# Performance work log

Hardware: AMD Instinct MI355X
Metric: run time of the kernel (lower is better)

## Reference

```python
import jax, jax.numpy as jnp
import numpy as np

B, S, D = 2, 2048, 1024
N_EXP, TOP_K = 8, 2
CAP_FACTOR = 1.25

def setup_inputs() -> dict:
    key = jax.random.key(0)
    k1, k2 = jax.random.split(key)
    x = jax.random.normal(k1, (B, S, D), dtype=jnp.float32)
    W_gate = jax.random.normal(k2, (N_EXP, D), dtype=jnp.float32) * (1.0 / np.sqrt(D))
    return {"x": x, "W_gate": W_gate}

def reference(x, W_gate):
    Bq, Sq, d = x.shape
    N = Bq * Sq                      # num_tokens
    n_exp = W_gate.shape[0]
    top_k = TOP_K
    cap = int(N * top_k * CAP_FACTOR / n_exp)  # exp_capacity (static)

    x_flat = x.reshape(N, d)
    logits = x_flat @ W_gate.T                      # [N, n_exp]
    top_vals, top_idx = jax.lax.top_k(logits, top_k)  # [N, k]
    gates = jax.nn.softmax(top_vals, axis=-1)       # [N, k]

    # Serial token-major, k-minor assignment order == flatten row-major.
    e_flat = top_idx.reshape(-1)                    # [N*k]
    oh = jax.nn.one_hot(e_flat, n_exp, dtype=jnp.int32)
    # position within expert = # earlier slots routed to same expert
    pos = (jnp.cumsum(oh, axis=0) - oh)[jnp.arange(N * top_k), e_flat]
    pos_safe = jnp.where(pos < cap, pos, cap)       # cap -> out-of-bounds -> dropped

    tok = jnp.arange(N * top_k) // top_k            # owning token per slot
    g_flat = gates.reshape(-1)

    exp_mask = jnp.zeros((N, n_exp, cap), jnp.float32)
    exp_mask = exp_mask.at[tok, e_flat, pos_safe].set(g_flat, mode='drop')

    exp_batches = jnp.zeros((n_exp, cap, d), jnp.float32)
    exp_batches = exp_batches.at[e_flat, pos_safe].set(x_flat[tok], mode='drop')

    return gates, exp_mask, exp_batches
```

## Files before the change

kernel.cpp:

```cpp
#include <hip/hip_runtime.h>
#include <math.h>

#define NTOK   4096
#define DIM    1024
#define NEXP   8
#define CAP    1280

#define OUT_MASK_OFF   ((size_t)NTOK*2)
#define OUT_BATCH_OFF  (OUT_MASK_OFF + (size_t)NTOK*NEXP*CAP)

typedef float f4 __attribute__((ext_vector_type(4)));

__global__ __launch_bounds__(256) void gate_kernel(
    const float* __restrict__ x, const float* __restrict__ Wg,
    float* __restrict__ gates_out,
    int* __restrict__ e0a, int* __restrict__ e1a,
    float* __restrict__ g0a, float* __restrict__ g1a)
{
    const int wave = threadIdx.x >> 6;
    const int lane = threadIdx.x & 63;
    const int t    = blockIdx.x * 4 + wave;

    const f4* xr = (const f4*)(x + (size_t)t * DIM);
    f4 xv[4];
#pragma unroll
    for (int p = 0; p < 4; ++p) xv[p] = xr[p * 64 + lane];

    float acc[NEXP];
#pragma unroll
    for (int e = 0; e < NEXP; ++e) {
        const f4* wr = (const f4*)(Wg + (size_t)e * DIM);
        float a = 0.f;
#pragma unroll
        for (int p = 0; p < 4; ++p) {
            const f4 w = wr[p * 64 + lane];
            a += xv[p].x * w.x + xv[p].y * w.y + xv[p].z * w.z + xv[p].w * w.w;
        }
        acc[e] = a;
    }

#pragma unroll
    for (int off = 32; off >= 1; off >>= 1) {
#pragma unroll
        for (int e = 0; e < NEXP; ++e)
            acc[e] += __shfl_xor(acc[e], off);
    }

    if (lane == 0) {
        float best = -INFINITY, second = -INFINITY;
        int b0 = 0, b1 = 0;
#pragma unroll
        for (int e = 0; e < NEXP; ++e) {
            const float v = acc[e];
            if (v > best)        { second = best; b1 = b0; best = v; b0 = e; }
            else if (v > second) { second = v; b1 = e; }
        }
        const float e1v = __expf(second - best);
        const float inv = 1.0f / (1.0f + e1v);
        const float g0 = inv, g1 = e1v * inv;

        gates_out[(size_t)t * 2]     = g0;
        gates_out[(size_t)t * 2 + 1] = g1;
        e0a[t] = b0; e1a[t] = b1;
        g0a[t] = g0; g1a[t] = g1;
    }
}

__global__ __launch_bounds__(256) void scan_kernel(
    const int* __restrict__ e0a, const int* __restrict__ e1a,
    int* __restrict__ pos0a, int* __restrict__ pos1a,
    int* __restrict__ inv_out)
{
    __shared__ int invs[NEXP * CAP];
    __shared__ unsigned wtot[4][4];

    const int tid  = threadIdx.x;
    const int wave = tid >> 6;
    const int lane = tid & 63;

    for (int i = tid; i < NEXP * CAP; i += 256) invs[i] = -1;

    const int tok0 = tid * 16;
    int ea[16], eb[16];
    {
        const int4* va = (const int4*)(e0a + tok0);
        const int4* vb = (const int4*)(e1a + tok0);
#pragma unroll
        for (int q = 0; q < 4; ++q) {
            int4 a = va[q], b = vb[q];
            ea[4*q] = a.x; ea[4*q+1] = a.y; ea[4*q+2] = a.z; ea[4*q+3] = a.w;
            eb[4*q] = b.x; eb[4*q+1] = b.y; eb[4*q+2] = b.z; eb[4*q+3] = b.w;
        }
    }

    int local[NEXP];
#pragma unroll
    for (int e = 0; e < NEXP; ++e) local[e] = 0;
#pragma unroll
    for (int j = 0; j < 16; ++j) { local[ea[j]]++; local[eb[j]]++; }

    unsigned pk[4];
#pragma unroll
    for (int q = 0; q < 4; ++q)
        pk[q] = (unsigned)local[2*q] | ((unsigned)local[2*q+1] << 16);
    const unsigned my0 = pk[0], my1 = pk[1], my2 = pk[2], my3 = pk[3];

#pragma unroll
    for (int off = 1; off < 64; off <<= 1) {
        unsigned n0 = __shfl_up((int)pk[0], off);
        unsigned n1 = __shfl_up((int)pk[1], off);
        unsigned n2 = __shfl_up((int)pk[2], off);
        unsigned n3 = __shfl_up((int)pk[3], off);
        if (lane >= off) { pk[0] += n0; pk[1] += n1; pk[2] += n2; pk[3] += n3; }
    }

    if (lane == 63) {
#pragma unroll
        for (int q = 0; q < 4; ++q) wtot[wave][q] = pk[q];
    }
    __syncthreads();

#pragma unroll
    for (int w = 0; w < 4; ++w) {
        if (w < wave) {
            pk[0] += wtot[w][0]; pk[1] += wtot[w][1];
            pk[2] += wtot[w][2]; pk[3] += wtot[w][3];
        }
    }
    pk[0] -= my0; pk[1] -= my1; pk[2] -= my2; pk[3] -= my3;

    int run[NEXP];
#pragma unroll
    for (int q = 0; q < 4; ++q) {
        run[2*q]   = (int)(pk[q] & 0xFFFFu);
        run[2*q+1] = (int)(pk[q] >> 16);
    }

    int p0r[16], p1r[16];
#pragma unroll
    for (int j = 0; j < 16; ++j) {
        const int tok = tok0 + j;
        int e = ea[j];
        int p = run[e]++;
        p0r[j] = p;
        if (p < CAP) invs[e * CAP + p] = tok;
        e = eb[j];
        p = run[e]++;
        p1r[j] = p;
        if (p < CAP) invs[e * CAP + p] = tok;
    }

#pragma unroll
    for (int q = 0; q < 4; ++q) {
        ((int4*)(pos0a + tok0))[q] = make_int4(p0r[4*q], p0r[4*q+1], p0r[4*q+2], p0r[4*q+3]);
        ((int4*)(pos1a + tok0))[q] = make_int4(p1r[4*q], p1r[4*q+1], p1r[4*q+2], p1r[4*q+3]);
    }
    __syncthreads();

    for (int i = tid; i < NEXP * CAP / 4; i += 256)
        ((int4*)inv_out)[i] = ((const int4*)invs)[i];
}

#define BATCH_BLOCKS 2560
__global__ __launch_bounds__(256) void writer_kernel(
    const int* __restrict__ e0a, const int* __restrict__ e1a,
    const int* __restrict__ pos0a, const int* __restrict__ pos1a,
    const float* __restrict__ g0a, const float* __restrict__ g1a,
    const int* __restrict__ inv, const float* __restrict__ x,
    float* __restrict__ mask_out, float* __restrict__ batch_out)
{
    const int tid = threadIdx.x;

    if (blockIdx.x < BATCH_BLOCKS) {
        const int4 tk = ((const int4*)inv)[blockIdx.x];
        const int toks[4] = { tk.x, tk.y, tk.z, tk.w };
        const int base = blockIdx.x * 4;
#pragma unroll
        for (int i = 0; i < 4; ++i) {
            const int tok = toks[i];
            f4 v = (f4)(0.f);
            if (tok >= 0)
                v = ((const f4*)(x + (size_t)tok * DIM))[tid];
            __builtin_nontemporal_store(v, (f4*)(batch_out + (size_t)(base + i) * DIM) + tid);
        }
    } else {
        const int t = (blockIdx.x - BATCH_BLOCKS) * 256 + tid;
        const int e0 = e0a[t], e1 = e1a[t];
        const int p0 = pos0a[t], p1 = pos1a[t];

        float* row = mask_out + (size_t)t * NEXP * CAP;
        if (p0 < CAP) row[e0 * CAP + p0] = g0a[t];
        if (p1 < CAP) row[e1 * CAP + p1] = g1a[t];
    }
}

extern "C" void kernel_launch(void* const* d_in, const int* in_sizes, int n_in,
                              void* d_out, int out_size, void* d_ws, size_t ws_size,
                              hipStream_t stream)
{
    const float* x  = (const float*)d_in[0];
    const float* Wg = (const float*)d_in[1];

    float* out   = (float*)d_out;
    float* gates = out;
    float* mask  = out + OUT_MASK_OFF;
    float* batch = out + OUT_BATCH_OFF;

    int* wsi = (int*)d_ws;
    int*   e0a  = wsi;
    int*   e1a  = wsi + NTOK;
    float* g0a  = (float*)(wsi + 2 * NTOK);
    float* g1a  = (float*)(wsi + 3 * NTOK);
    int*   p0a  = wsi + 4 * NTOK;
    int*   p1a  = wsi + 5 * NTOK;
    int*   inv  = wsi + 6 * NTOK;

    hipMemsetAsync(mask, 0, (size_t)NTOK * NEXP * CAP * sizeof(float), stream);

    gate_kernel  <<<NTOK / 4, 256, 0, stream>>>(x, Wg, gates, e0a, e1a, g0a, g1a);
    scan_kernel  <<<1, 256, 0, stream>>>(e0a, e1a, p0a, p1a, inv);
    writer_kernel<<<BATCH_BLOCKS + 16, 256, 0, stream>>>(
        e0a, e1a, p0a, p1a, g0a, g1a, inv, x, mask, batch);
}
```

Baseline: 229.4 us.

## Fuse mask zeroing into gate kernel and scatter gates from scan kernel

Drops the separate hipMemsetAsync over the large expert mask (about 168 MB) and instead has each gate block zero its slice of the mask with nontemporal vector stores, alongside its gating dot products. The single-block scan kernel now writes the gate values straight into the mask, so the position arrays and the mask branch of the writer kernel go away. This removes one launch and a round trip of the position arrays. The cost is that 16 scattered-store iterations now run serially in one block, and the gate kernel's compute is mixed with a heavy store stream.

New measurement: 239.8 us. 1.05x slower.

```diff
diff --git a/kernel.cpp b/kernel.cpp
--- a/kernel.cpp
+++ b/kernel.cpp
@@ -9,17 +9,31 @@
 #define OUT_MASK_OFF   ((size_t)NTOK*2)
 #define OUT_BATCH_OFF  (OUT_MASK_OFF + (size_t)NTOK*NEXP*CAP)
 
+#define MASK_F4        ((NTOK * NEXP * CAP) / 4)
+#define GATE_BLOCKS    (NTOK / 4)
+#define MASK_F4_PER_BLK (MASK_F4 / GATE_BLOCKS)
+
 typedef float f4 __attribute__((ext_vector_type(4)));
 
-__global__ __launch_bounds__(256) void gate_kernel(
+__global__ __launch_bounds__(256) void gate_zero_kernel(
     const float* __restrict__ x, const float* __restrict__ Wg,
     float* __restrict__ gates_out,
     int* __restrict__ e0a, int* __restrict__ e1a,
-    float* __restrict__ g0a, float* __restrict__ g1a)
-{
-    const int wave = threadIdx.x >> 6;
-    const int lane = threadIdx.x & 63;
+    float* __restrict__ g0a, float* __restrict__ g1a,
+    float* __restrict__ mask_out)
+{
+    const int tid  = threadIdx.x;
+    const int wave = tid >> 6;
+    const int lane = tid & 63;
     const int t    = blockIdx.x * 4 + wave;
+
+    {
+        f4 z = (f4)(0.f);
+        f4* mz = (f4*)mask_out + (size_t)blockIdx.x * MASK_F4_PER_BLK;
+#pragma unroll
+        for (int i = 0; i < MASK_F4_PER_BLK / 256; ++i)
+            __builtin_nontemporal_store(z, mz + i * 256 + tid);
+    }
 
     const f4* xr = (const f4*)(x + (size_t)t * DIM);
     f4 xv[4];
@@ -66,10 +80,10 @@
     }
 }
 
-__global__ __launch_bounds__(256) void scan_kernel(
+__global__ __launch_bounds__(256) void scan_scatter_kernel(
     const int* __restrict__ e0a, const int* __restrict__ e1a,
-    int* __restrict__ pos0a, int* __restrict__ pos1a,
-    int* __restrict__ inv_out)
+    const float* __restrict__ g0a, const float* __restrict__ g1a,
+    float* __restrict__ mask_out, int* __restrict__ inv_out)
 {
     __shared__ int invs[NEXP * CAP];
     __shared__ unsigned wtot[4][4];
@@ -82,14 +96,20 @@
 
     const int tok0 = tid * 16;
     int ea[16], eb[16];
+    float ga[16], gb[16];
     {
         const int4* va = (const int4*)(e0a + tok0);
         const int4* vb = (const int4*)(e1a + tok0);
+        const f4*   vg = (const f4*)(g0a + tok0);
+        const f4*   vh = (const f4*)(g1a + tok0);
 #pragma unroll
         for (int q = 0; q < 4; ++q) {
             int4 a = va[q], b = vb[q];
             ea[4*q] = a.x; ea[4*q+1] = a.y; ea[4*q+2] = a.z; ea[4*q+3] = a.w;
             eb[4*q] = b.x; eb[4*q+1] = b.y; eb[4*q+2] = b.z; eb[4*q+3] = b.w;
+            f4 g = vg[q], h = vh[q];
+            ga[4*q] = g.x; ga[4*q+1] = g.y; ga[4*q+2] = g.z; ga[4*q+3] = g.w;
+            gb[4*q] = h.x; gb[4*q+1] = h.y; gb[4*q+2] = h.z; gb[4*q+3] = h.w;
         }
     }
 
@@ -136,24 +156,16 @@
         run[2*q+1] = (int)(pk[q] >> 16);
     }
 
-    int p0r[16], p1r[16];
 #pragma unroll
     for (int j = 0; j < 16; ++j) {
         const int tok = tok0 + j;
+        float* row = mask_out + (size_t)tok * NEXP * CAP;
         int e = ea[j];
         int p = run[e]++;
-        p0r[j] = p;
-        if (p < CAP) invs[e * CAP + p] = tok;
+        if (p < CAP) { invs[e * CAP + p] = tok; row[e * CAP + p] = ga[j]; }
         e = eb[j];
         p = run[e]++;
-        p1r[j] = p;
-        if (p < CAP) invs[e * CAP + p] = tok;
-    }
-
-#pragma unroll
-    for (int q = 0; q < 4; ++q) {
-        ((int4*)(pos0a + tok0))[q] = make_int4(p0r[4*q], p0r[4*q+1], p0r[4*q+2], p0r[4*q+3]);
-        ((int4*)(pos1a + tok0))[q] = make_int4(p1r[4*q], p1r[4*q+1], p1r[4*q+2], p1r[4*q+3]);
+        if (p < CAP) { invs[e * CAP + p] = tok; row[e * CAP + p] = gb[j]; }
     }
     __syncthreads();
 
@@ -162,35 +174,21 @@
 }
 
 #define BATCH_BLOCKS 2560
-__global__ __launch_bounds__(256) void writer_kernel(
-    const int* __restrict__ e0a, const int* __restrict__ e1a,
-    const int* __restrict__ pos0a, const int* __restrict__ pos1a,
-    const float* __restrict__ g0a, const float* __restrict__ g1a,
+__global__ __launch_bounds__(256) void batch_kernel(
     const int* __restrict__ inv, const float* __restrict__ x,
-    float* __restrict__ mask_out, float* __restrict__ batch_out)
+    float* __restrict__ batch_out)
 {
     const int tid = threadIdx.x;
-
-    if (blockIdx.x < BATCH_BLOCKS) {
-        const int4 tk = ((const int4*)inv)[blockIdx.x];
-        const int toks[4] = { tk.x, tk.y, tk.z, tk.w };
-        const int base = blockIdx.x * 4;
-#pragma unroll
-        for (int i = 0; i < 4; ++i) {
-            const int tok = toks[i];
-            f4 v = (f4)(0.f);
-            if (tok >= 0)
-                v = ((const f4*)(x + (size_t)tok * DIM))[tid];
-            __builtin_nontemporal_store(v, (f4*)(batch_out + (size_t)(base + i) * DIM) + tid);
-        }
-    } else {
-        const int t = (blockIdx.x - BATCH_BLOCKS) * 256 + tid;
-        const int e0 = e0a[t], e1 = e1a[t];
-        const int p0 = pos0a[t], p1 = pos1a[t];
-
-        float* row = mask_out + (size_t)t * NEXP * CAP;
-        if (p0 < CAP) row[e0 * CAP + p0] = g0a[t];
-        if (p1 < CAP) row[e1 * CAP + p1] = g1a[t];
+    const int4 tk = ((const int4*)inv)[blockIdx.x];
+    const int toks[4] = { tk.x, tk.y, tk.z, tk.w };
+    const int base = blockIdx.x * 4;
+#pragma unroll
+    for (int i = 0; i < 4; ++i) {
+        const int tok = toks[i];
+        f4 v = (f4)(0.f);
+        if (tok >= 0)
+            v = ((const f4*)(x + (size_t)tok * DIM))[tid];
+        __builtin_nontemporal_store(v, (f4*)(batch_out + (size_t)(base + i) * DIM) + tid);
     }
 }
 
@@ -211,14 +209,10 @@
     int*   e1a  = wsi + NTOK;
     float* g0a  = (float*)(wsi + 2 * NTOK);
     float* g1a  = (float*)(wsi + 3 * NTOK);
-    int*   p0a  = wsi + 4 * NTOK;
-    int*   p1a  = wsi + 5 * NTOK;
-    int*   inv  = wsi + 6 * NTOK;
-
-    hipMemsetAsync(mask, 0, (size_t)NTOK * NEXP * CAP * sizeof(float), stream);
-
-    gate_kernel  <<<NTOK / 4, 256, 0, stream>>>(x, Wg, gates, e0a, e1a, g0a, g1a);
-    scan_kernel  <<<1, 256, 0, stream>>>(e0a, e1a, p0a, p1a, inv);
-    writer_kernel<<<BATCH_BLOCKS + 16, 256, 0, stream>>>(
-        e0a, e1a, p0a, p1a, g0a, g1a, inv, x, mask, batch);
-}
+    int*   inv  = wsi + 4 * NTOK;
+
+    gate_zero_kernel  <<<GATE_BLOCKS, 256, 0, stream>>>(
+        x, Wg, gates, e0a, e1a, g0a, g1a, mask);
+    scan_scatter_kernel<<<1, 256, 0, stream>>>(e0a, e1a, g0a, g1a, mask, inv);
+    batch_kernel      <<<BATCH_BLOCKS, 256, 0, stream>>>(inv, x, batch);
+}
```
